# Optimization experiments

Hardware: AMD Instinct MI355X
Metric: run time of the kernel (lower is better)

Reference implementation:

```python
import jax, jax.numpy as jnp
import numpy as np
import math

B, NG0, E = 4, 2500, 100000        # graphs, nodes/graph, total edges
H, C = 2, 512                      # heads, hidden channels
DIM_IN = 512
RATIO, NEG = 0.7, 0.2              # pooling ratio, leaky_relu slope

def _ks():
    ks, n = [], NG0
    for _ in range(4):
        n = math.ceil(RATIO * n)
        ks.append(n)
    return ks
KS = _ks()  # [1750, 1225, 858, 601]


def setup_inputs() -> dict:
    key = jax.random.key(0)
    k = jax.random.split(key, 12)
    Eper = E // B
    src_l = jax.random.randint(k[0], (B, Eper), 0, NG0, dtype=jnp.int32)
    off = jax.random.randint(k[10], (B, Eper), 1, NG0, dtype=jnp.int32)
    dst_l = (src_l + off) % NG0  # no self loops (GATv2 adds its own)
    goff = (jnp.arange(B, dtype=jnp.int32) * NG0)[:, None]
    edge_index = jnp.stack([(src_l + goff).reshape(-1), (dst_l + goff).reshape(-1)])
    sc = 1.0 / np.sqrt(C)
    return {
        "x": jax.random.normal(k[1], (B * NG0, DIM_IN), jnp.float32),
        "edge_index": edge_index,
        "gat_Wl": jax.random.normal(k[2], (4, C, H * C), jnp.float32) * sc,
        "gat_bl": jnp.zeros((4, H * C), jnp.float32),
        "gat_Wr": jax.random.normal(k[3], (4, C, H * C), jnp.float32) * sc,
        "gat_br": jnp.zeros((4, H * C), jnp.float32),
        "gat_att": jax.random.normal(k[4], (4, H, C), jnp.float32) * sc,
        "gat_bias": jnp.zeros((4, C), jnp.float32),
        "sag_Wrel": jax.random.normal(k[5], (4, C), jnp.float32) * sc,
        "sag_brel": jnp.zeros((4,), jnp.float32),
        "sag_Wroot": jax.random.normal(k[6], (4, C), jnp.float32) * sc,
        "W1": jax.random.normal(k[7], (2 * C, C), jnp.float32) / np.sqrt(2 * C),
        "b1": jnp.zeros((C,), jnp.float32),
        "W2": jax.random.normal(k[8], (C, C // 2), jnp.float32) * sc,
        "b2": jnp.zeros((C // 2,), jnp.float32),
        "W3": jax.random.normal(k[9], (C // 2, 5), jnp.float32) / np.sqrt(C // 2),
        "b3": jnp.zeros((5,), jnp.float32),
    }


def _gatv2(x, src, dst, emask, Wl, bl, Wr, br, att, bias):
    """GATv2Conv(concat=False): mean over heads, self-loops added."""
    N = x.shape[0]
    loop = jnp.arange(N, dtype=src.dtype)
    s = jnp.concatenate([src, loop])
    d = jnp.concatenate([dst, loop])
    m = jnp.concatenate([emask, jnp.ones((N,), bool)])
    xl = (x @ Wl + bl).reshape(N, H, C)   # source transform
    xr = (x @ Wr + br).reshape(N, H, C)   # target transform
    e = jax.nn.leaky_relu(xl[s] + xr[d], NEG)          # [E', H, C]
    logit = jnp.einsum('ehc,hc->eh', e, att)
    logit = jnp.where(m[:, None], logit, -1e9)
    mx = jax.ops.segment_max(logit, d, num_segments=N)  # segment softmax
    p = jnp.where(m[:, None], jnp.exp(logit - mx[d]), 0.0)
    den = jax.ops.segment_sum(p, d, num_segments=N)
    alpha = p / jnp.maximum(den[d], 1e-16)
    out = jax.ops.segment_sum(xl[s] * alpha[..., None], d, num_segments=N)
    return out.mean(axis=1) + bias


def _sagpool(x, src, dst, emask, Wrel, brel, Wroot, k, ng):
    """SAGPooling with GraphConv scorer, tanh nonlinearity, multiplier=1."""
    N = x.shape[0]
    agg = jax.ops.segment_sum(jnp.where(emask[:, None], x[src], 0.0), dst, num_segments=N)
    score = agg @ Wrel + brel + x @ Wroot               # [N]
    topv, topi = jax.lax.top_k(score.reshape(B, ng), k)  # per-graph top-k
    glob = (jnp.arange(B, dtype=jnp.int32)[:, None] * ng + topi.astype(jnp.int32)).reshape(-1)
    xnew = x[glob] * jnp.tanh(topv).reshape(-1, 1)
    newidx = jnp.full((N,), -1, jnp.int32).at[glob].set(jnp.arange(B * k, dtype=jnp.int32))
    ns, nd = newidx[src], newidx[dst]
    nmask = emask & (ns >= 0) & (nd >= 0)               # filter_adj via mask
    return xnew, jnp.where(nmask, ns, 0), jnp.where(nmask, nd, 0), nmask


def reference(x, edge_index, gat_Wl, gat_bl, gat_Wr, gat_br, gat_att, gat_bias,
              sag_Wrel, sag_brel, sag_Wroot, W1, b1, W2, b2, W3, b3):
    src, dst = edge_index[0], edge_index[1]
    emask = jnp.ones((E,), bool)
    ng = NG0
    readout = 0.0
    for i in range(4):
        x = jax.nn.relu(_gatv2(x, src, dst, emask, gat_Wl[i], gat_bl[i],
                               gat_Wr[i], gat_br[i], gat_att[i], gat_bias[i]))
        x, src, dst, emask = _sagpool(x, src, dst, emask, sag_Wrel[i],
                                      sag_brel[i], sag_Wroot[i], KS[i], ng)
        ng = KS[i]
        xg = x.reshape(B, ng, C)
        readout = readout + jnp.concatenate([xg.max(axis=1), xg.mean(axis=1)], axis=1)
    h = jax.nn.relu(readout @ W1 + b1)   # dropout p=0.2 is identity in eval
    h = jax.nn.relu(h @ W2 + b2)
    logits = h @ W3 + b3
    return logits, jax.nn.softmax(logits, axis=1)
```

## Files before the change

### kernel.cpp

```cpp
#include <hip/hip_runtime.h>
#include <math.h>

#define NB   4
#define NG0  2500
#define ETOT 100000
#define CH   512
#define NEGS 0.2f
#define BCAP 64

static const int h_Ns[5]  = {10000, 7000, 4900, 3432, 2404};
static const int h_ngs[4] = {2500, 1750, 1225, 858};
static const int h_ks[4]  = {1750, 1225, 858, 601};

typedef __bf16 bf16x8 __attribute__((ext_vector_type(8)));
typedef __bf16 bf16x4 __attribute__((ext_vector_type(4)));
typedef float  f32x4  __attribute__((ext_vector_type(4)));

#define GLOAD16(g, l)                                                              \
    __builtin_amdgcn_global_load_lds(                                              \
        (const __attribute__((address_space(1))) unsigned int*)(g),                \
        (__attribute__((address_space(3))) unsigned int*)(l), 16, 0, 0)

__global__ void k_init_build(const int* __restrict__ ei, int* src, int* dst, int* mask,
                             int* cnt, int* bucket) {
    int e = blockIdx.x * blockDim.x + threadIdx.x;
    if (e >= ETOT) return;
    int s = ei[e], d = ei[ETOT + e];
    src[e] = s; dst[e] = d; mask[e] = 1;
    int p = atomicAdd(&cnt[d], 1);
    if (p < BCAP) bucket[(d << 6) + p] = s;
}

__global__ void k_remap_build(int* src, int* dst, int* mask, const int* __restrict__ newidx,
                              int* cnt, int* bucket) {
    int e = blockIdx.x * blockDim.x + threadIdx.x;
    if (e >= ETOT) return;
    if (!mask[e]) return;
    int ns = newidx[src[e]];
    int nd = newidx[dst[e]];
    if (ns >= 0 && nd >= 0) {
        src[e] = ns; dst[e] = nd;
        int p = atomicAdd(&cnt[nd], 1);
        if (p < BCAP) bucket[(nd << 6) + p] = ns;
    } else mask[e] = 0;
}

__global__ void k_cvtA(const float* __restrict__ x, __bf16* __restrict__ hi,
                       __bf16* __restrict__ lo, int n) {
    int i = (blockIdx.x * blockDim.x + threadIdx.x) * 8;
    if (i >= n) return;
    float4 a = *(const float4*)(x + i);
    float4 b = *(const float4*)(x + i + 4);
    float f[8] = {a.x, a.y, a.z, a.w, b.x, b.y, b.z, b.w};
    bf16x8 vh, vl;
#pragma unroll
    for (int j = 0; j < 8; ++j) {
        __bf16 h = (__bf16)f[j];
        vh[j] = h;
        vl[j] = (__bf16)(f[j] - (float)h);
    }
    *(bf16x8*)(hi + i) = vh;
    *(bf16x8*)(lo + i) = vl;
}

__global__ void k_cvtWt(const float* __restrict__ gWl, const float* __restrict__ gWr,
                        __bf16* __restrict__ WtH, __bf16* __restrict__ WtL) {
    int m = blockIdx.z;
    const float* src = ((m & 1) ? gWr : gWl) + (size_t)(m >> 1) * 512 * 1024;
    __bf16* oh = WtH + (size_t)m * 1024 * 512;
    __bf16* ol = WtL + (size_t)m * 1024 * 512;
    int nb = blockIdx.x * 32, kb = blockIdx.y * 32;
    __shared__ float tile[32][33];
#pragma unroll
    for (int j = 0; j < 4; ++j) {
        int kk = threadIdx.y + j * 8;
        tile[kk][threadIdx.x] = src[(size_t)(kb + kk) * 1024 + nb + threadIdx.x];
    }
    __syncthreads();
#pragma unroll
    for (int j = 0; j < 4; ++j) {
        int nn = threadIdx.y + j * 8;
        float v = tile[threadIdx.x][nn];
        __bf16 h = (__bf16)v;
        __bf16 l = (__bf16)(v - (float)h);
        oh[(size_t)(nb + nn) * 512 + kb + threadIdx.x] = h;
        ol[(size_t)(nb + nn) * 512 + kb + threadIdx.x] = l;
    }
}

__global__ void k_transpose(const float* __restrict__ src, float* __restrict__ dst, int R, int C) {
    __shared__ float tile[32][33];
    int rb = blockIdx.y * 32, cb = blockIdx.x * 32;
#pragma unroll
    for (int j = 0; j < 4; ++j) {
        int r = rb + threadIdx.y + j * 8;
        int c = cb + threadIdx.x;
        if (r < R && c < C) tile[threadIdx.y + j * 8][threadIdx.x] = src[(size_t)r * C + c];
    }
    __syncthreads();
#pragma unroll
    for (int j = 0; j < 4; ++j) {
        int c = cb + threadIdx.y + j * 8;
        int r = rb + threadIdx.x;
        if (r < R && c < C) dst[(size_t)c * R + r] = tile[threadIdx.x][threadIdx.y + j * 8];
    }
}

__global__ void k_prep_bias(const float* __restrict__ gbl, const float* __restrict__ gbr,
                            float* __restrict__ biasC) {
    int i = blockIdx.x * blockDim.x + threadIdx.x;
    if (i >= 4 * 2048) return;
    int l = i >> 11, c = i & 2047;
    biasC[i] = (c < 1024) ? gbl[l * 1024 + c] : gbr[l * 1024 + c - 1024];
}

__global__ __launch_bounds__(256) void k_gemm3(const __bf16* __restrict__ Ah, const __bf16* __restrict__ Al,
                                               const __bf16* __restrict__ Bh, const __bf16* __restrict__ Bl,
                                               const float* __restrict__ bias, float* __restrict__ out,
                                               int M, int ldo) {
    __shared__ __bf16 sAh[128 * 32];
    __shared__ __bf16 sAl[128 * 32];
    __shared__ __bf16 sBh[128 * 32];
    __shared__ __bf16 sBl[128 * 32];
    int tid = threadIdx.x;
    int nRows = (M + 127) >> 7;
    int pid = blockIdx.x;
    int fullG = nRows >> 3;
    int inFull = fullG << 7;
    int rowT, colT;
    if (pid < inFull) {
        int g = pid >> 7, r = pid & 127;
        rowT = (g << 3) + (r & 7);
        colT = r >> 3;
    } else {
        int r = pid - inFull;
        int tail = nRows - (fullG << 3);
        rowT = (fullG << 3) + r % tail;
        colT = r / tail;
    }
    int rowBase = rowT << 7, colBase = colT << 7;
    int wave = tid >> 6, lane = tid & 63;
    int wr = (wave >> 1) * 64, wc = (wave & 1) * 64;
    f32x4 acc[4][4];
#pragma unroll
    for (int a = 0; a < 4; ++a)
#pragma unroll
        for (int b = 0; b < 4; ++b) { acc[a][b][0] = 0.f; acc[a][b][1] = 0.f; acc[a][b][2] = 0.f; acc[a][b][3] = 0.f; }

    int srow0 = tid >> 2;
    int ps = tid & 3;
    auto stage = [&](int k0) {
#pragma unroll
        for (int c = 0; c < 2; ++c) {
            int row = (c << 6) + srow0;
            int ls = ps ^ ((row >> 1) & 3);
            int ldsoff = c * 2048 + tid * 8;
            int grA = rowBase + row; if (grA >= M) grA = M - 1;
            int gnB = colBase + row;
            const __bf16* gah = Ah + (size_t)grA * 512 + k0 + ls * 8;
            const __bf16* gal = Al + (size_t)grA * 512 + k0 + ls * 8;
            const __bf16* gbh = Bh + (size_t)gnB * 512 + k0 + ls * 8;
            const __bf16* gbl2 = Bl + (size_t)gnB * 512 + k0 + ls * 8;
            GLOAD16(gah, &sAh[ldsoff]);
            GLOAD16(gal, &sAl[ldsoff]);
            GLOAD16(gbh, &sBh[ldsoff]);
            GLOAD16(gbl2, &sBl[ldsoff]);
        }
    };

    int fl = lane & 15, g = lane >> 4;
    stage(0);
    __syncthreads();
    for (int ks = 0; ks < 16; ++ks) {
        bf16x8 afh[4], afl[4], bfh[4], bfl[4];
#pragma unroll
        for (int fr = 0; fr < 4; ++fr) {
            int r = wr + fr * 16 + fl;
            int po = (g ^ ((r >> 1) & 3)) << 3;
            afh[fr] = *(const bf16x8*)&sAh[r * 32 + po];
            afl[fr] = *(const bf16x8*)&sAl[r * 32 + po];
        }
#pragma unroll
        for (int fc = 0; fc < 4; ++fc) {
            int cc = wc + fc * 16 + fl;
            int po = (g ^ ((cc >> 1) & 3)) << 3;
            bfh[fc] = *(const bf16x8*)&sBh[cc * 32 + po];
            bfl[fc] = *(const bf16x8*)&sBl[cc * 32 + po];
        }
        __syncthreads();
        if (ks < 15) stage((ks + 1) * 32);
#pragma unroll
        for (int fr = 0; fr < 4; ++fr) {
#pragma unroll
            for (int fc = 0; fc < 4; ++fc) {
                acc[fr][fc] = __builtin_amdgcn_mfma_f32_16x16x32_bf16(afh[fr], bfh[fc], acc[fr][fc], 0, 0, 0);
                acc[fr][fc] = __builtin_amdgcn_mfma_f32_16x16x32_bf16(afh[fr], bfl[fc], acc[fr][fc], 0, 0, 0);
                acc[fr][fc] = __builtin_amdgcn_mfma_f32_16x16x32_bf16(afl[fr], bfh[fc], acc[fr][fc], 0, 0, 0);
            }
        }
        __syncthreads();
    }
    int orow0 = rowBase + wr + 4 * (lane >> 4);
    int ocol0 = colBase + wc + fl;
#pragma unroll
    for (int fr = 0; fr < 4; ++fr) {
#pragma unroll
        for (int fc = 0; fc < 4; ++fc) {
            int col = ocol0 + fc * 16;
            float bv = bias[col];
#pragma unroll
            for (int j = 0; j < 4; ++j) {
                int row = orow0 + fr * 16 + j;
                if (row < M) out[(size_t)row * ldo + col] = acc[fr][fc][j] + bv;
            }
        }
    }
}

__global__ __launch_bounds__(256) void k_gat_wave(const float* __restrict__ xlr,
                                                  const int* __restrict__ cnt,
                                                  const int* __restrict__ bucket,
                                                  const float* __restrict__ att,
                                                  const float* __restrict__ bias,
                                                  const float* __restrict__ Wrel,
                                                  const float* __restrict__ Wroot,
                                                  float* __restrict__ out,
                                                  float* __restrict__ y0, float* __restrict__ y1, int N) {
    int d = (blockIdx.x * blockDim.x + threadIdx.x) >> 6;
    if (d >= N) return;
    int lane = threadIdx.x & 63;
    int c0 = lane * 16;
    const float* xrp = xlr + (size_t)d * 2048 + 1024 + c0;
    float4 xr0 = *(const float4*)(xrp + 0), xr1 = *(const float4*)(xrp + 4);
    float4 xr2 = *(const float4*)(xrp + 8), xr3 = *(const float4*)(xrp + 12);
    const float* atp = att + c0;
    float4 at0 = *(const float4*)(atp + 0), at1 = *(const float4*)(atp + 4);
    float4 at2 = *(const float4*)(atp + 8), at3 = *(const float4*)(atp + 12);
    float acc[16];
    float m, den;
    {
        const float* xsp = xlr + (size_t)d * 2048 + c0;
        float4 v0 = *(const float4*)(xsp + 0), v1 = *(const float4*)(xsp + 4);
        float4 v2 = *(const float4*)(xsp + 8), v3 = *(const float4*)(xsp + 12);
        float p = 0.f, e;
        e = v0.x + xr0.x; e = e > 0.f ? e : NEGS * e; p += e * at0.x;
        e = v0.y + xr0.y; e = e > 0.f ? e : NEGS * e; p += e * at0.y;
        e = v0.z + xr0.z; e = e > 0.f ? e : NEGS * e; p += e * at0.z;
        e = v0.w + xr0.w; e = e > 0.f ? e : NEGS * e; p += e * at0.w;
        e = v1.x + xr1.x; e = e > 0.f ? e : NEGS * e; p += e * at1.x;
        e = v1.y + xr1.y; e = e > 0.f ? e : NEGS * e; p += e * at1.y;
        e = v1.z + xr1.z; e = e > 0.f ? e : NEGS * e; p += e * at1.z;
        e = v1.w + xr1.w; e = e > 0.f ? e : NEGS * e; p += e * at1.w;
        e = v2.x + xr2.x; e = e > 0.f ? e : NEGS * e; p += e * at2.x;
        e = v2.y + xr2.y; e = e > 0.f ? e : NEGS * e; p += e * at2.y;
        e = v2.z + xr2.z; e = e > 0.f ? e : NEGS * e; p += e * at2.z;
        e = v2.w + xr2.w; e = e > 0.f ? e : NEGS * e; p += e * at2.w;
        e = v3.x + xr3.x; e = e > 0.f ? e : NEGS * e; p += e * at3.x;
        e = v3.y + xr3.y; e = e > 0.f ? e : NEGS * e; p += e * at3.y;
        e = v3.z + xr3.z; e = e > 0.f ? e : NEGS * e; p += e * at3.z;
        e = v3.w + xr3.w; e = e > 0.f ? e : NEGS * e; p += e * at3.w;
#pragma unroll
        for (int o = 1; o <= 16; o <<= 1) p += __shfl_xor(p, o, 64);
        m = p; den = 1.f;
        acc[0] = v0.x; acc[1] = v0.y; acc[2] = v0.z; acc[3] = v0.w;
        acc[4] = v1.x; acc[5] = v1.y; acc[6] = v1.z; acc[7] = v1.w;
        acc[8] = v2.x; acc[9] = v2.y; acc[10] = v2.z; acc[11] = v2.w;
        acc[12] = v3.x; acc[13] = v3.y; acc[14] = v3.z; acc[15] = v3.w;
    }
    int rs = d << 6, re = rs + cnt[d];
    for (int eidx = rs; eidx < re; ++eidx) {
        int s = bucket[eidx];
        const float* xsp = xlr + (size_t)s * 2048 + c0;
        float4 v0 = *(const float4*)(xsp + 0), v1 = *(const float4*)(xsp + 4);
        float4 v2 = *(const float4*)(xsp + 8), v3 = *(const float4*)(xsp + 12);
        float p = 0.f, e;
        e = v0.x + xr0.x; e = e > 0.f ? e : NEGS * e; p += e * at0.x;
        e = v0.y + xr0.y; e = e > 0.f ? e : NEGS * e; p += e * at0.y;
        e = v0.z + xr0.z; e = e > 0.f ? e : NEGS * e; p += e * at0.z;
        e = v0.w + xr0.w; e = e > 0.f ? e : NEGS * e; p += e * at0.w;
        e = v1.x + xr1.x; e = e > 0.f ? e : NEGS * e; p += e * at1.x;
        e = v1.y + xr1.y; e = e > 0.f ? e : NEGS * e; p += e * at1.y;
        e = v1.z + xr1.z; e = e > 0.f ? e : NEGS * e; p += e * at1.z;
        e = v1.w + xr1.w; e = e > 0.f ? e : NEGS * e; p += e * at1.w;
        e = v2.x + xr2.x; e = e > 0.f ? e : NEGS * e; p += e * at2.x;
        e = v2.y + xr2.y; e = e > 0.f ? e : NEGS * e; p += e * at2.y;
        e = v2.z + xr2.z; e = e > 0.f ? e : NEGS * e; p += e * at2.z;
        e = v2.w + xr2.w; e = e > 0.f ? e : NEGS * e; p += e * at2.w;
        e = v3.x + xr3.x; e = e > 0.f ? e : NEGS * e; p += e * at3.x;
        e = v3.y + xr3.y; e = e > 0.f ? e : NEGS * e; p += e * at3.y;
        e = v3.z + xr3.z; e = e > 0.f ? e : NEGS * e; p += e * at3.z;
        e = v3.w + xr3.w; e = e > 0.f ? e : NEGS * e; p += e * at3.w;
#pragma unroll
        for (int o = 1; o <= 16; o <<= 1) p += __shfl_xor(p, o, 64);
        float nm = fmaxf(m, p);
        float sc = __expf(m - nm);
        float w = __expf(p - nm);
        m = nm;
        den = den * sc + w;
        acc[0] = acc[0] * sc + w * v0.x; acc[1] = acc[1] * sc + w * v0.y;
        acc[2] = acc[2] * sc + w * v0.z; acc[3] = acc[3] * sc + w * v0.w;
        acc[4] = acc[4] * sc + w * v1.x; acc[5] = acc[5] * sc + w * v1.y;
        acc[6] = acc[6] * sc + w * v1.z; acc[7] = acc[7] * sc + w * v1.w;
        acc[8] = acc[8] * sc + w * v2.x; acc[9] = acc[9] * sc + w * v2.y;
        acc[10] = acc[10] * sc + w * v2.z; acc[11] = acc[11] * sc + w * v2.w;
        acc[12] = acc[12] * sc + w * v3.x; acc[13] = acc[13] * sc + w * v3.y;
        acc[14] = acc[14] * sc + w * v3.z; acc[15] = acc[15] * sc + w * v3.w;
    }
    float inv = 1.f / fmaxf(den, 1e-16f);
    float o16[16];
#pragma unroll
    for (int j = 0; j < 16; ++j) {
        float a = acc[j] * inv;
        float b = __shfl_xor(a, 32, 64);
        o16[j] = 0.5f * (a + b);
    }
    float s0 = 0.f, s1 = 0.f;
    if (lane < 32) {
        const float* bp = bias + c0;
        const float* wa = Wrel + c0;
        const float* wb = Wroot + c0;
        float* op = out + (size_t)d * 512 + c0;
#pragma unroll
        for (int j = 0; j < 16; j += 4) {
            float4 bb = *(const float4*)(bp + j);
            float4 va = *(const float4*)(wa + j);
            float4 vb = *(const float4*)(wb + j);
            float4 r;
            r.x = fmaxf(o16[j + 0] + bb.x, 0.f);
            r.y = fmaxf(o16[j + 1] + bb.y, 0.f);
            r.z = fmaxf(o16[j + 2] + bb.z, 0.f);
            r.w = fmaxf(o16[j + 3] + bb.w, 0.f);
            *(float4*)(op + j) = r;
            s0 += r.x * va.x + r.y * va.y + r.z * va.z + r.w * va.w;
            s1 += r.x * vb.x + r.y * vb.y + r.z * vb.z + r.w * vb.w;
        }
    }
#pragma unroll
    for (int o = 16; o > 0; o >>= 1) {
        s0 += __shfl_xor(s0, o, 64);
        s1 += __shfl_xor(s1, o, 64);
    }
    if (lane == 0) { y0[d] = s0; y1[d] = s1; }
}

__global__ void k_score2(const float* __restrict__ y0, const float* __restrict__ y1,
                         const int* __restrict__ cnt, const int* __restrict__ bucket,
                         const float* __restrict__ brel_p,
                         float* __restrict__ score, int N) {
    int d = blockIdx.x * blockDim.x + threadIdx.x;
    if (d >= N) return;
    float s = y1[d] + brel_p[0];
    int rs = d << 6, re = rs + cnt[d];
    for (int e = rs; e < re; ++e) s += y0[bucket[e]];
    score[d] = s;
}

__global__ __launch_bounds__(256) void k_topk_radix(const float* __restrict__ score, int ng, int k,
                                                    int* __restrict__ newidx, int* __restrict__ sel_old,
                                                    float* __restrict__ sel_scale) {
    int b = blockIdx.x;
    int t = threadIdx.x;
    __shared__ unsigned int keys[NG0];
    __shared__ int hist[256];
    __shared__ int scnt[256];
    __shared__ unsigned int s_pref, s_amask;
    __shared__ int s_krem, s_gt;
    for (int i = t; i < ng; i += 256) {
        float f = score[b * ng + i];
        unsigned int u = __float_as_uint(f);
        u = (u & 0x80000000u) ? ~u : (u | 0x80000000u);
        keys[i] = u;
        newidx[b * ng + i] = -1;
    }
    if (t == 0) { s_pref = 0u; s_amask = 0u; s_krem = k; s_gt = 0; }
    __syncthreads();
    for (int pass = 0; pass < 4; ++pass) {
        int shift = 24 - 8 * pass;
        hist[t] = 0;
        __syncthreads();
        unsigned int amask = s_amask, pref = s_pref;
        for (int i = t; i < ng; i += 256) {
            unsigned int u = keys[i];
            if ((u & amask) == pref) atomicAdd(&hist[(u >> shift) & 255], 1);
        }
        __syncthreads();
        if (t == 0) {
            int krem = s_krem, cum = 0, dsel = 0;
            for (int dd = 255; dd >= 0; --dd) {
                cum += hist[dd];
                if (cum >= krem) { dsel = dd; krem -= (cum - hist[dd]); break; }
            }
            s_pref = s_pref | ((unsigned int)dsel << shift);
            s_amask = s_amask | (0xFFu << shift);
            s_krem = krem;
        }
        __syncthreads();
    }
    unsigned int T = s_pref;
    int krem = s_krem;
    int chunk = (ng + 255) / 256;
    int lo = t * chunk, hi = min(ng, lo + chunk);
    int ceq = 0;
    for (int i = lo; i < hi; ++i) if (keys[i] == T) ceq++;
    scnt[t] = ceq;
    __syncthreads();
    for (int o = 1; o < 256; o <<= 1) {
        int add = (t >= o) ? scnt[t - o] : 0;
        __syncthreads();
        scnt[t] += add;
        __syncthreads();
    }
    int eq_rank = scnt[t] - ceq;
    for (int i = lo; i < hi; ++i) {
        unsigned int u = keys[i];
        int slot = -1;
        if (u > T) slot = atomicAdd(&s_gt, 1);
        else if (u == T) {
            if (eq_rank < krem) slot = (k - krem) + eq_rank;
            eq_rank++;
        }
        if (slot >= 0) {
            int oldg = b * ng + i;
            int newg = b * k + slot;
            newidx[oldg] = newg;
            sel_old[newg] = oldg;
            sel_scale[newg] = tanhf(score[oldg]);
        }
    }
}

__global__ __launch_bounds__(128) void k_pool_cvt(const float* __restrict__ x, const int* __restrict__ sel_old,
                                                  const float* __restrict__ sel_scale, float* __restrict__ xn,
                                                  __bf16* __restrict__ hi, __bf16* __restrict__ lo,
                                                  int* __restrict__ cnt) {
    int nn = blockIdx.x;
    if (threadIdx.x == 0) cnt[nn] = 0;
    int so = sel_old[nn];
    float sc = sel_scale[nn];
    int c = threadIdx.x * 4;
    float4 vv = *(const float4*)(x + (size_t)so * 512 + c);
    vv.x *= sc; vv.y *= sc; vv.z *= sc; vv.w *= sc;
    *(float4*)(xn + (size_t)nn * 512 + c) = vv;
    float f[4] = {vv.x, vv.y, vv.z, vv.w};
    bf16x4 vh, vl;
#pragma unroll
    for (int j = 0; j < 4; ++j) {
        __bf16 hh = (__bf16)f[j];
        vh[j] = hh;
        vl[j] = (__bf16)(f[j] - (float)hh);
    }
    *(bf16x4*)(hi + (size_t)nn * 512 + c) = vh;
    *(bf16x4*)(lo + (size_t)nn * 512 + c) = vl;
}

__global__ __launch_bounds__(256) void k_readout_part(const float* __restrict__ x, int k,
                                                      float* __restrict__ pmax, float* __restrict__ psum) {
    int b = blockIdx.x, cg = blockIdx.y, rc = blockIdx.z;
    int t = threadIdx.x;
    int c4 = (t & 63);
    int rl = t >> 6;
    int col = cg * 256 + c4 * 4;
    int rstart = rc * 4 + rl;
    float4 mx = make_float4(-1e30f, -1e30f, -1e30f, -1e30f);
    float4 sm = make_float4(0.f, 0.f, 0.f, 0.f);
    for (int j = rstart; j < k; j += 32) {
        float4 v = *(const float4*)(x + ((size_t)(b * k + j)) * 512 + col);
        mx.x = fmaxf(mx.x, v.x); mx.y = fmaxf(mx.y, v.y); mx.z = fmaxf(mx.z, v.z); mx.w = fmaxf(mx.w, v.w);
        sm.x += v.x; sm.y += v.y; sm.z += v.z; sm.w += v.w;
    }
    __shared__ float lmx[256 * 4];
    __shared__ float lsm[256 * 4];
    int li = c4 * 4 + rl * 256;
    lmx[li + 0] = mx.x; lmx[li + 1] = mx.y; lmx[li + 2] = mx.z; lmx[li + 3] = mx.w;
    lsm[li + 0] = sm.x; lsm[li + 1] = sm.y; lsm[li + 2] = sm.z; lsm[li + 3] = sm.w;
    __syncthreads();
    if (rl == 0) {
        int ci = c4 * 4;
#pragma unroll
        for (int q = 0; q < 4; ++q) {
            float m = fmaxf(fmaxf(lmx[ci + q], lmx[ci + q + 256]), fmaxf(lmx[ci + q + 512], lmx[ci + q + 768]));
            float s = lsm[ci + q] + lsm[ci + q + 256] + lsm[ci + q + 512] + lsm[ci + q + 768];
            size_t o = ((size_t)(b * 8 + rc)) * 512 + col + q;
            pmax[o] = m;
            psum[o] = s;
        }
    }
}

__global__ __launch_bounds__(512) void k_readout_fin(const float* __restrict__ pmax, const float* __restrict__ psum,
                                                     int k, float* __restrict__ readout) {
    int b = blockIdx.x;
    int c = threadIdx.x;
    float m = -1e30f, s = 0.f;
#pragma unroll
    for (int rc = 0; rc < 8; ++rc) {
        size_t o = ((size_t)(b * 8 + rc)) * 512 + c;
        m = fmaxf(m, pmax[o]);
        s += psum[o];
    }
    readout[b * 1024 + c] += m;
    readout[b * 1024 + 512 + c] += s / (float)k;
}

__global__ __launch_bounds__(256) void k_mlp1(const float* __restrict__ readout, const float* __restrict__ W1t,
                                              const float* __restrict__ b1, float* __restrict__ h1) {
    int wid = (blockIdx.x * blockDim.x + threadIdx.x) >> 6;
    int lane = threadIdx.x & 63;
    int b = wid >> 9, col = wid & 511;
    const float* rp = readout + b * 1024 + lane * 16;
    const float* wp = W1t + (size_t)col * 1024 + lane * 16;
    float s = 0.f;
#pragma unroll
    for (int j = 0; j < 4; ++j) {
        float4 v = *(const float4*)(rp + j * 4);
        float4 w = *(const float4*)(wp + j * 4);
        s += v.x * w.x + v.y * w.y + v.z * w.z + v.w * w.w;
    }
#pragma unroll
    for (int o = 32; o > 0; o >>= 1) s += __shfl_xor(s, o, 64);
    if (lane == 0) h1[b * 512 + col] = fmaxf(s + b1[col], 0.f);
}

__global__ __launch_bounds__(256) void k_mlp2(const float* __restrict__ h1, const float* __restrict__ W2t,
                                              const float* __restrict__ b2, float* __restrict__ h2) {
    int wid = (blockIdx.x * blockDim.x + threadIdx.x) >> 6;
    int lane = threadIdx.x & 63;
    int b = wid >> 8, col = wid & 255;
    const float* hp = h1 + b * 512 + lane * 8;
    const float* wp = W2t + (size_t)col * 512 + lane * 8;
    float s = 0.f;
#pragma unroll
    for (int j = 0; j < 2; ++j) {
        float4 v = *(const float4*)(hp + j * 4);
        float4 w = *(const float4*)(wp + j * 4);
        s += v.x * w.x + v.y * w.y + v.z * w.z + v.w * w.w;
    }
#pragma unroll
    for (int o = 32; o > 0; o >>= 1) s += __shfl_xor(s, o, 64);
    if (lane == 0) h2[b * 256 + col] = fmaxf(s + b2[col], 0.f);
}

__global__ __launch_bounds__(256) void k_mlp3(const float* __restrict__ h2, const float* __restrict__ W3,
                                              const float* __restrict__ b3, float* __restrict__ out) {
    int b = threadIdx.x >> 6;
    int lane = threadIdx.x & 63;
    float hv[4];
    int idx[4];
#pragma unroll
    for (int j = 0; j < 4; ++j) { idx[j] = lane + j * 64; hv[j] = h2[b * 256 + idx[j]]; }
    float lg[5];
#pragma unroll
    for (int q = 0; q < 5; ++q) {
        float p = 0.f;
#pragma unroll
        for (int j = 0; j < 4; ++j) p += hv[j] * W3[idx[j] * 5 + q];
#pragma unroll
        for (int o = 32; o > 0; o >>= 1) p += __shfl_xor(p, o, 64);
        lg[q] = p + b3[q];
    }
    if (lane == 0) {
        float m = lg[0];
#pragma unroll
        for (int q = 1; q < 5; ++q) m = fmaxf(m, lg[q]);
        float den = 0.f;
#pragma unroll
        for (int q = 0; q < 5; ++q) den += __expf(lg[q] - m);
#pragma unroll
        for (int q = 0; q < 5; ++q) {
            out[b * 5 + q] = lg[q];
            out[NB * 5 + b * 5 + q] = __expf(lg[q] - m) / den;
        }
    }
}

extern "C" void kernel_launch(void* const* d_in, const int* in_sizes, int n_in,
                              void* d_out, int out_size, void* d_ws, size_t ws_size,
                              hipStream_t stream) {
    const float* x0    = (const float*)d_in[0];
    const int*   ei    = (const int*)d_in[1];
    const float* gWl   = (const float*)d_in[2];
    const float* gbl   = (const float*)d_in[3];
    const float* gWr   = (const float*)d_in[4];
    const float* gbr   = (const float*)d_in[5];
    const float* gatt  = (const float*)d_in[6];
    const float* gbias = (const float*)d_in[7];
    const float* sWrel = (const float*)d_in[8];
    const float* sbrel = (const float*)d_in[9];
    const float* sWroot= (const float*)d_in[10];
    const float* W1 = (const float*)d_in[11];
    const float* b1 = (const float*)d_in[12];
    const float* W2 = (const float*)d_in[13];
    const float* b2 = (const float*)d_in[14];
    const float* W3 = (const float*)d_in[15];
    const float* b3 = (const float*)d_in[16];
    float* out = (float*)d_out;

    char* base = (char*)d_ws;
    size_t off = 0;
    auto alloc = [&](size_t bytes) -> void* {
        void* p = base + off;
        off += (bytes + 255) & ~(size_t)255;
        return p;
    };
    int*   s_src   = (int*)alloc((size_t)ETOT * 4);
    int*   s_dst   = (int*)alloc((size_t)ETOT * 4);
    int*   s_mask  = (int*)alloc((size_t)ETOT * 4);
    int*   bucket  = (int*)alloc((size_t)h_Ns[0] * BCAP * 4);
    int*   cnt     = (int*)alloc((size_t)(h_Ns[0] + 1) * 4);
    float* score   = (float*)alloc((size_t)h_Ns[0] * 4);
    int*   newidx  = (int*)alloc((size_t)h_Ns[0] * 4);
    int*   sel_old = (int*)alloc((size_t)7000 * 4);
    float* sel_scale = (float*)alloc((size_t)7000 * 4);
    float* readout = (float*)alloc((size_t)NB * 1024 * 4);
    float* pmax    = (float*)alloc((size_t)NB * 8 * 512 * 4);
    float* psum    = (float*)alloc((size_t)NB * 8 * 512 * 4);
    float* y0      = (float*)alloc((size_t)h_Ns[0] * 4);
    float* y1      = (float*)alloc((size_t)h_Ns[0] * 4);
    float* xlr     = (float*)alloc((size_t)h_Ns[0] * 2048 * 4);
    float* gatout  = (float*)alloc((size_t)h_Ns[0] * 512 * 4);
    float* xpool   = (float*)alloc((size_t)7000 * 512 * 4);
    __bf16* Ah     = (__bf16*)alloc((size_t)h_Ns[0] * 512 * 2);
    __bf16* Al     = (__bf16*)alloc((size_t)h_Ns[0] * 512 * 2);
    __bf16* WtH    = (__bf16*)alloc((size_t)8 * 1024 * 512 * 2);
    __bf16* WtL    = (__bf16*)alloc((size_t)8 * 1024 * 512 * 2);
    float* biasC   = (float*)alloc((size_t)4 * 2048 * 4);
    float* W1t     = (float*)alloc((size_t)512 * 1024 * 4);
    float* W2t     = (float*)alloc((size_t)256 * 512 * 4);
    float* h1b     = (float*)alloc((size_t)NB * 512 * 4);
    float* h2b     = (float*)alloc((size_t)NB * 256 * 4);

    hipMemsetAsync(readout, 0, (size_t)NB * 1024 * 4, stream);
    hipMemsetAsync(cnt, 0, (size_t)(h_Ns[0] + 1) * 4, stream);
    k_cvtWt<<<dim3(32, 16, 8), dim3(32, 8), 0, stream>>>(gWl, gWr, WtH, WtL);
    k_cvtA<<<(h_Ns[0] * 512 / 8 + 255) / 256, 256, 0, stream>>>(x0, Ah, Al, h_Ns[0] * 512);
    k_prep_bias<<<(4 * 2048 + 255) / 256, 256, 0, stream>>>(gbl, gbr, biasC);
    k_transpose<<<dim3(16, 32), dim3(32, 8), 0, stream>>>(W1, W1t, 1024, 512);
    k_transpose<<<dim3(8, 16), dim3(32, 8), 0, stream>>>(W2, W2t, 512, 256);

    for (int i = 0; i < 4; ++i) {
        int N = h_Ns[i], ng = h_ngs[i], k = h_ks[i];
        if (i == 0)
            k_init_build<<<(ETOT + 255) / 256, 256, 0, stream>>>(ei, s_src, s_dst, s_mask, cnt, bucket);
        else
            k_remap_build<<<(ETOT + 255) / 256, 256, 0, stream>>>(s_src, s_dst, s_mask, newidx, cnt, bucket);
        int nRows = (N + 127) >> 7;
        k_gemm3<<<nRows * 16, 256, 0, stream>>>(Ah, Al, WtH + (size_t)(2 * i) * 1024 * 512, WtL + (size_t)(2 * i) * 1024 * 512,
                                                biasC + (size_t)i * 2048, xlr, N, 2048);
        k_gat_wave<<<(N + 3) / 4, 256, 0, stream>>>(xlr, cnt, bucket, gatt + (size_t)i * 1024,
                                                    gbias + (size_t)i * 512, sWrel + (size_t)i * 512,
                                                    sWroot + (size_t)i * 512, gatout, y0, y1, N);
        k_score2<<<(N + 255) / 256, 256, 0, stream>>>(y0, y1, cnt, bucket, sbrel + i, score, N);
        k_topk_radix<<<NB, 256, 0, stream>>>(score, ng, k, newidx, sel_old, sel_scale);
        k_pool_cvt<<<NB * k, 128, 0, stream>>>(gatout, sel_old, sel_scale, xpool, Ah, Al, cnt);
        k_readout_part<<<dim3(NB, 2, 8), 256, 0, stream>>>(xpool, k, pmax, psum);
        k_readout_fin<<<NB, 512, 0, stream>>>(pmax, psum, k, readout);
    }
    k_mlp1<<<512, 256, 0, stream>>>(readout, W1t, b1, h1b);
    k_mlp2<<<256, 256, 0, stream>>>(h1b, W2t, b2, h2b);
    k_mlp3<<<1, 256, 0, stream>>>(h2b, W3, b3, out);
}
```

Measured before the change: 715.8 us.

## Unroll GAT edge loop by two, parallelize radix select scan, fuse pool with readout

The GAT aggregation loop now handles two neighbour edges per iteration, so two gather streams and their reductions can overlap and the online-softmax rescale runs once per pair. The serial digit search done by thread 0 in the radix top-k is replaced by a block-wide prefix scan. The pooling/bf16-conversion kernel and the readout partial kernel become one launch that reads the selected rows straight from the GAT output, so the pooled buffer no longer has to be written and read back. The costs are higher register pressure in the GAT kernel and an extra indirect gather per element in the readout path.

New measurement: 644.5 us. -10.0%, faster.

```diff
diff --git a/kernel.cpp b/kernel.cpp
--- a/kernel.cpp
+++ b/kernel.cpp
@@ -217,6 +217,23 @@
     }
 }
 
+__device__ __forceinline__ float gat_row(const float* __restrict__ xsp,
+                                         const float* xr, const float* at, float* v) {
+    float p = 0.f;
+#pragma unroll
+    for (int j = 0; j < 16; j += 4) {
+        float4 vv = *(const float4*)(xsp + j);
+        v[j + 0] = vv.x; v[j + 1] = vv.y; v[j + 2] = vv.z; v[j + 3] = vv.w;
+    }
+#pragma unroll
+    for (int j = 0; j < 16; ++j) {
+        float e = v[j] + xr[j];
+        e = e > 0.f ? e : NEGS * e;
+        p += e * at[j];
+    }
+    return p;
+}
+
 __global__ __launch_bounds__(256) void k_gat_wave(const float* __restrict__ xlr,
                                                   const int* __restrict__ cnt,
                                                   const int* __restrict__ bucket,
@@ -230,81 +247,59 @@
     if (d >= N) return;
     int lane = threadIdx.x & 63;
     int c0 = lane * 16;
-    const float* xrp = xlr + (size_t)d * 2048 + 1024 + c0;
-    float4 xr0 = *(const float4*)(xrp + 0), xr1 = *(const float4*)(xrp + 4);
-    float4 xr2 = *(const float4*)(xrp + 8), xr3 = *(const float4*)(xrp + 12);
-    const float* atp = att + c0;
-    float4 at0 = *(const float4*)(atp + 0), at1 = *(const float4*)(atp + 4);
-    float4 at2 = *(const float4*)(atp + 8), at3 = *(const float4*)(atp + 12);
-    float acc[16];
-    float m, den;
+    float xr[16], at[16];
+#pragma unroll
+    for (int j = 0; j < 16; j += 4) {
+        float4 a = *(const float4*)(xlr + (size_t)d * 2048 + 1024 + c0 + j);
+        xr[j + 0] = a.x; xr[j + 1] = a.y; xr[j + 2] = a.z; xr[j + 3] = a.w;
+        float4 b = *(const float4*)(att + c0 + j);
+        at[j + 0] = b.x; at[j + 1] = b.y; at[j + 2] = b.z; at[j + 3] = b.w;
+    }
+    float acc[16], m, den;
     {
-        const float* xsp = xlr + (size_t)d * 2048 + c0;
-        float4 v0 = *(const float4*)(xsp + 0), v1 = *(const float4*)(xsp + 4);
-        float4 v2 = *(const float4*)(xsp + 8), v3 = *(const float4*)(xsp + 12);
-        float p = 0.f, e;
-        e = v0.x + xr0.x; e = e > 0.f ? e : NEGS * e; p += e * at0.x;
-        e = v0.y + xr0.y; e = e > 0.f ? e : NEGS * e; p += e * at0.y;
-        e = v0.z + xr0.z; e = e > 0.f ? e : NEGS * e; p += e * at0.z;
-        e = v0.w + xr0.w; e = e > 0.f ? e : NEGS * e; p += e * at0.w;
-        e = v1.x + xr1.x; e = e > 0.f ? e : NEGS * e; p += e * at1.x;
-        e = v1.y + xr1.y; e = e > 0.f ? e : NEGS * e; p += e * at1.y;
-        e = v1.z + xr1.z; e = e > 0.f ? e : NEGS * e; p += e * at1.z;
-        e = v1.w + xr1.w; e = e > 0.f ? e : NEGS * e; p += e * at1.w;
-        e = v2.x + xr2.x; e = e > 0.f ? e : NEGS * e; p += e * at2.x;
-        e = v2.y + xr2.y; e = e > 0.f ? e : NEGS * e; p += e * at2.y;
-        e = v2.z + xr2.z; e = e > 0.f ? e : NEGS * e; p += e * at2.z;
-        e = v2.w + xr2.w; e = e > 0.f ? e : NEGS * e; p += e * at2.w;
-        e = v3.x + xr3.x; e = e > 0.f ? e : NEGS * e; p += e * at3.x;
-        e = v3.y + xr3.y; e = e > 0.f ? e : NEGS * e; p += e * at3.y;
-        e = v3.z + xr3.z; e = e > 0.f ? e : NEGS * e; p += e * at3.z;
-        e = v3.w + xr3.w; e = e > 0.f ? e : NEGS * e; p += e * at3.w;
+        float v[16];
+        float p = gat_row(xlr + (size_t)d * 2048 + c0, xr, at, v);
 #pragma unroll
         for (int o = 1; o <= 16; o <<= 1) p += __shfl_xor(p, o, 64);
         m = p; den = 1.f;
-        acc[0] = v0.x; acc[1] = v0.y; acc[2] = v0.z; acc[3] = v0.w;
-        acc[4] = v1.x; acc[5] = v1.y; acc[6] = v1.z; acc[7] = v1.w;
-        acc[8] = v2.x; acc[9] = v2.y; acc[10] = v2.z; acc[11] = v2.w;
-        acc[12] = v3.x; acc[13] = v3.y; acc[14] = v3.z; acc[15] = v3.w;
-    }
-    int rs = d << 6, re = rs + cnt[d];
-    for (int eidx = rs; eidx < re; ++eidx) {
-        int s = bucket[eidx];
-        const float* xsp = xlr + (size_t)s * 2048 + c0;
-        float4 v0 = *(const float4*)(xsp + 0), v1 = *(const float4*)(xsp + 4);
-        float4 v2 = *(const float4*)(xsp + 8), v3 = *(const float4*)(xsp + 12);
-        float p = 0.f, e;
-        e = v0.x + xr0.x; e = e > 0.f ? e : NEGS * e; p += e * at0.x;
-        e = v0.y + xr0.y; e = e > 0.f ? e : NEGS * e; p += e * at0.y;
-        e = v0.z + xr0.z; e = e > 0.f ? e : NEGS * e; p += e * at0.z;
-        e = v0.w + xr0.w; e = e > 0.f ? e : NEGS * e; p += e * at0.w;
-        e = v1.x + xr1.x; e = e > 0.f ? e : NEGS * e; p += e * at1.x;
-        e = v1.y + xr1.y; e = e > 0.f ? e : NEGS * e; p += e * at1.y;
-        e = v1.z + xr1.z; e = e > 0.f ? e : NEGS * e; p += e * at1.z;
-        e = v1.w + xr1.w; e = e > 0.f ? e : NEGS * e; p += e * at1.w;
-        e = v2.x + xr2.x; e = e > 0.f ? e : NEGS * e; p += e * at2.x;
-        e = v2.y + xr2.y; e = e > 0.f ? e : NEGS * e; p += e * at2.y;
-        e = v2.z + xr2.z; e = e > 0.f ? e : NEGS * e; p += e * at2.z;
-        e = v2.w + xr2.w; e = e > 0.f ? e : NEGS * e; p += e * at2.w;
-        e = v3.x + xr3.x; e = e > 0.f ? e : NEGS * e; p += e * at3.x;
-        e = v3.y + xr3.y; e = e > 0.f ? e : NEGS * e; p += e * at3.y;
-        e = v3.z + xr3.z; e = e > 0.f ? e : NEGS * e; p += e * at3.z;
-        e = v3.w + xr3.w; e = e > 0.f ? e : NEGS * e; p += e * at3.w;
-#pragma unroll
-        for (int o = 1; o <= 16; o <<= 1) p += __shfl_xor(p, o, 64);
-        float nm = fmaxf(m, p);
+#pragma unroll
+        for (int j = 0; j < 16; ++j) acc[j] = v[j];
+    }
+    int rs = d << 6;
+    int re = rs + cnt[d];
+    int e = rs;
+    for (; e + 1 < re; e += 2) {
+        int s1 = bucket[e], s2 = bucket[e + 1];
+        float v1[16], v2[16];
+        float p1 = gat_row(xlr + (size_t)s1 * 2048 + c0, xr, at, v1);
+        float p2 = gat_row(xlr + (size_t)s2 * 2048 + c0, xr, at, v2);
+#pragma unroll
+        for (int o = 1; o <= 16; o <<= 1) {
+            p1 += __shfl_xor(p1, o, 64);
+            p2 += __shfl_xor(p2, o, 64);
+        }
+        float nm = fmaxf(m, fmaxf(p1, p2));
         float sc = __expf(m - nm);
-        float w = __expf(p - nm);
+        float w1 = __expf(p1 - nm);
+        float w2 = __expf(p2 - nm);
         m = nm;
-        den = den * sc + w;
-        acc[0] = acc[0] * sc + w * v0.x; acc[1] = acc[1] * sc + w * v0.y;
-        acc[2] = acc[2] * sc + w * v0.z; acc[3] = acc[3] * sc + w * v0.w;
-        acc[4] = acc[4] * sc + w * v1.x; acc[5] = acc[5] * sc + w * v1.y;
-        acc[6] = acc[6] * sc + w * v1.z; acc[7] = acc[7] * sc + w * v1.w;
-        acc[8] = acc[8] * sc + w * v2.x; acc[9] = acc[9] * sc + w * v2.y;
-        acc[10] = acc[10] * sc + w * v2.z; acc[11] = acc[11] * sc + w * v2.w;
-        acc[12] = acc[12] * sc + w * v3.x; acc[13] = acc[13] * sc + w * v3.y;
-        acc[14] = acc[14] * sc + w * v3.z; acc[15] = acc[15] * sc + w * v3.w;
+        den = den * sc + w1 + w2;
+#pragma unroll
+        for (int j = 0; j < 16; ++j) acc[j] = (acc[j] * sc + w1 * v1[j]) + w2 * v2[j];
+    }
+    if (e < re) {
+        int s1 = bucket[e];
+        float v1[16];
+        float p1 = gat_row(xlr + (size_t)s1 * 2048 + c0, xr, at, v1);
+#pragma unroll
+        for (int o = 1; o <= 16; o <<= 1) p1 += __shfl_xor(p1, o, 64);
+        float nm = fmaxf(m, p1);
+        float sc = __expf(m - nm);
+        float w1 = __expf(p1 - nm);
+        m = nm;
+        den = den * sc + w1;
+#pragma unroll
+        for (int j = 0; j < 16; ++j) acc[j] = acc[j] * sc + w1 * v1[j];
     }
     float inv = 1.f / fmaxf(den, 1e-16f);
     float o16[16];
@@ -314,7 +309,7 @@
         float b = __shfl_xor(a, 32, 64);
         o16[j] = 0.5f * (a + b);
     }
-    float s0 = 0.f, s1 = 0.f;
+    float s0 = 0.f, s1v = 0.f;
     if (lane < 32) {
         const float* bp = bias + c0;
         const float* wa = Wrel + c0;
@@ -332,15 +327,17 @@
             r.w = fmaxf(o16[j + 3] + bb.w, 0.f);
             *(float4*)(op + j) = r;
             s0 += r.x * va.x + r.y * va.y + r.z * va.z + r.w * va.w;
-            s1 += r.x * vb.x + r.y * vb.y + r.z * vb.z + r.w * vb.w;
+            s1v += r.x * vb.x + r.y * vb.y + r.z * vb.z + r.w * vb.w;
         }
     }
 #pragma unroll
     for (int o = 16; o > 0; o >>= 1) {
         s0 += __shfl_xor(s0, o, 64);
-        s1 += __shfl_xor(s1, o, 64);
-    }
-    if (lane == 0) { y0[d] = s0; y1[d] = s1; }
+        s1v += __shfl_xor(s1v, o, 64);
+    }
+    s0 += __shfl_xor(s0, 32, 64);
+    s1v += __shfl_xor(s1v, 32, 64);
+    if (lane == 0) { y0[d] = s0; y1[d] = s1v; }
 }
 
 __global__ void k_score2(const float* __restrict__ y0, const float* __restrict__ y1,
@@ -360,9 +357,11 @@
                                                     float* __restrict__ sel_scale) {
     int b = blockIdx.x;
     int t = threadIdx.x;
+    int lane = t & 63, wave = t >> 6;
     __shared__ unsigned int keys[NG0];
     __shared__ int hist[256];
     __shared__ int scnt[256];
+    __shared__ int wsum4[4];
     __shared__ unsigned int s_pref, s_amask;
     __shared__ int s_krem, s_gt;
     for (int i = t; i < ng; i += 256) {
@@ -379,20 +378,29 @@
         hist[t] = 0;
         __syncthreads();
         unsigned int amask = s_amask, pref = s_pref;
+        int krem_c = s_krem;
         for (int i = t; i < ng; i += 256) {
             unsigned int u = keys[i];
             if ((u & amask) == pref) atomicAdd(&hist[(u >> shift) & 255], 1);
         }
         __syncthreads();
-        if (t == 0) {
-            int krem = s_krem, cum = 0, dsel = 0;
-            for (int dd = 255; dd >= 0; --dd) {
-                cum += hist[dd];
-                if (cum >= krem) { dsel = dd; krem -= (cum - hist[dd]); break; }
-            }
-            s_pref = s_pref | ((unsigned int)dsel << shift);
-            s_amask = s_amask | (0xFFu << shift);
-            s_krem = krem;
+        int rh = hist[255 - t];
+        int x = rh;
+#pragma unroll
+        for (int o = 1; o < 64; o <<= 1) {
+            int y = __shfl_up(x, o, 64);
+            if (lane >= o) x += y;
+        }
+        if (lane == 63) wsum4[wave] = x;
+        __syncthreads();
+        int woff = 0;
+#pragma unroll
+        for (int wv = 0; wv < 3; ++wv) if (wave > wv) woff += wsum4[wv];
+        x += woff;
+        if (x >= krem_c && (x - rh) < krem_c) {
+            s_pref = pref | ((unsigned int)(255 - t) << shift);
+            s_amask = amask | (0xFFu << shift);
+            s_krem = krem_c - (x - rh);
         }
         __syncthreads();
     }
@@ -429,42 +437,51 @@
     }
 }
 
-__global__ __launch_bounds__(128) void k_pool_cvt(const float* __restrict__ x, const int* __restrict__ sel_old,
-                                                  const float* __restrict__ sel_scale, float* __restrict__ xn,
-                                                  __bf16* __restrict__ hi, __bf16* __restrict__ lo,
-                                                  int* __restrict__ cnt) {
-    int nn = blockIdx.x;
-    if (threadIdx.x == 0) cnt[nn] = 0;
-    int so = sel_old[nn];
-    float sc = sel_scale[nn];
-    int c = threadIdx.x * 4;
-    float4 vv = *(const float4*)(x + (size_t)so * 512 + c);
-    vv.x *= sc; vv.y *= sc; vv.z *= sc; vv.w *= sc;
-    *(float4*)(xn + (size_t)nn * 512 + c) = vv;
-    float f[4] = {vv.x, vv.y, vv.z, vv.w};
-    bf16x4 vh, vl;
-#pragma unroll
-    for (int j = 0; j < 4; ++j) {
-        __bf16 hh = (__bf16)f[j];
-        vh[j] = hh;
-        vl[j] = (__bf16)(f[j] - (float)hh);
-    }
-    *(bf16x4*)(hi + (size_t)nn * 512 + c) = vh;
-    *(bf16x4*)(lo + (size_t)nn * 512 + c) = vl;
-}
-
-__global__ __launch_bounds__(256) void k_readout_part(const float* __restrict__ x, int k,
+__global__ __launch_bounds__(256) void k_pool_readout(const float* __restrict__ gatout,
+                                                      const int* __restrict__ sel_old,
+                                                      const float* __restrict__ sel_scale,
+                                                      __bf16* __restrict__ hi, __bf16* __restrict__ lo,
+                                                      int* __restrict__ cnt, int k,
                                                       float* __restrict__ pmax, float* __restrict__ psum) {
-    int b = blockIdx.x, cg = blockIdx.y, rc = blockIdx.z;
+    int npoolb = (NB * k) >> 1;
+    int bid = blockIdx.x;
+    if (bid < npoolb) {
+        int nn = (bid << 1) + (threadIdx.x >> 7);
+        int t2 = threadIdx.x & 127;
+        if (t2 == 0) cnt[nn] = 0;
+        int so = sel_old[nn];
+        float sc = sel_scale[nn];
+        int c = t2 * 4;
+        float4 vv = *(const float4*)(gatout + (size_t)so * 512 + c);
+        vv.x *= sc; vv.y *= sc; vv.z *= sc; vv.w *= sc;
+        float f[4] = {vv.x, vv.y, vv.z, vv.w};
+        bf16x4 vh, vl;
+#pragma unroll
+        for (int j = 0; j < 4; ++j) {
+            __bf16 hh = (__bf16)f[j];
+            vh[j] = hh;
+            vl[j] = (__bf16)(f[j] - (float)hh);
+        }
+        *(bf16x4*)(hi + (size_t)nn * 512 + c) = vh;
+        *(bf16x4*)(lo + (size_t)nn * 512 + c) = vl;
+        return;
+    }
+    int rb = bid - npoolb;
+    int b = rb >> 4;
+    int cg = (rb >> 3) & 1;
+    int rc = rb & 7;
     int t = threadIdx.x;
-    int c4 = (t & 63);
+    int c4 = t & 63;
     int rl = t >> 6;
     int col = cg * 256 + c4 * 4;
     int rstart = rc * 4 + rl;
     float4 mx = make_float4(-1e30f, -1e30f, -1e30f, -1e30f);
     float4 sm = make_float4(0.f, 0.f, 0.f, 0.f);
     for (int j = rstart; j < k; j += 32) {
-        float4 v = *(const float4*)(x + ((size_t)(b * k + j)) * 512 + col);
+        int so = sel_old[b * k + j];
+        float sc = sel_scale[b * k + j];
+        float4 v = *(const float4*)(gatout + (size_t)so * 512 + col);
+        v.x *= sc; v.y *= sc; v.z *= sc; v.w *= sc;
         mx.x = fmaxf(mx.x, v.x); mx.y = fmaxf(mx.y, v.y); mx.z = fmaxf(mx.z, v.z); mx.w = fmaxf(mx.w, v.w);
         sm.x += v.x; sm.y += v.y; sm.z += v.z; sm.w += v.w;
     }
@@ -618,7 +635,6 @@
     float* y1      = (float*)alloc((size_t)h_Ns[0] * 4);
     float* xlr     = (float*)alloc((size_t)h_Ns[0] * 2048 * 4);
     float* gatout  = (float*)alloc((size_t)h_Ns[0] * 512 * 4);
-    float* xpool   = (float*)alloc((size_t)7000 * 512 * 4);
     __bf16* Ah     = (__bf16*)alloc((size_t)h_Ns[0] * 512 * 2);
     __bf16* Al     = (__bf16*)alloc((size_t)h_Ns[0] * 512 * 2);
     __bf16* WtH    = (__bf16*)alloc((size_t)8 * 1024 * 512 * 2);
@@ -651,8 +667,7 @@
                                                     sWroot + (size_t)i * 512, gatout, y0, y1, N);
         k_score2<<<(N + 255) / 256, 256, 0, stream>>>(y0, y1, cnt, bucket, sbrel + i, score, N);
         k_topk_radix<<<NB, 256, 0, stream>>>(score, ng, k, newidx, sel_old, sel_scale);
-        k_pool_cvt<<<NB * k, 128, 0, stream>>>(gatout, sel_old, sel_scale, xpool, Ah, Al, cnt);
-        k_readout_part<<<dim3(NB, 2, 8), 256, 0, stream>>>(xpool, k, pmax, psum);
+        k_pool_readout<<<(NB * k) / 2 + 64, 256, 0, stream>>>(gatout, sel_old, sel_scale, Ah, Al, cnt, k, pmax, psum);
         k_readout_fin<<<NB, 512, 0, stream>>>(pmax, psum, k, readout);
     }
     k_mlp1<<<512, 256, 0, stream>>>(readout, W1t, b1, h1b);
```
